# Performance work log

Measured on AMD Instinct MI355X. Metric: run time of the kernel, lower is better.

## Reference

```python
import jax, jax.numpy as jnp
import numpy as np

B, D, V, S = 16384, 768, 50257, 100


def setup_inputs() -> dict:
    key = jax.random.key(0)
    k1, k2, k3, k4, k5 = jax.random.split(key, 5)
    return {
        "predictions": jax.random.normal(k1, (B, D), dtype=jnp.float32),
        "labels": jax.random.randint(k2, (B,), 0, V, dtype=jnp.int64)
        if jax.config.jax_enable_x64 else jax.random.randint(k2, (B,), 0, V).astype(jnp.int32),
        "projection": jax.random.normal(k3, (V, D), dtype=jnp.float32) * 0.02,
        "bias": jax.random.normal(k4, (V,), dtype=jnp.float32) * 0.02,
        "samples": jax.random.randint(k5, (S,), 0, V).astype(jnp.int32),
    }


def reference(predictions, labels, projection, bias, samples):
    n_classes = projection.shape[0]
    num_sampling = samples.shape[0]
    # true-label scores: gather rows then rowwise dot  [B]
    label_scores = jnp.einsum("bd,bd->b", predictions, projection[labels]) + bias[labels]
    # noise scores vs sampled classes  [B, S]
    noise_scores = predictions @ projection[samples].T + bias[samples][None, :]
    noise_scores = noise_scores + jnp.log(jnp.float32(n_classes - 1))
    # reject accidental hits of the true label among samples
    reject = (labels[:, None] == samples[None, :]) & (labels[:, None] != -100)
    noise_scores = noise_scores - 1000000.0 * reject.astype(noise_scores.dtype)
    noise_scores = noise_scores - jnp.log(
        (num_sampling - reject.sum(-1, keepdims=True)).astype(jnp.float32)
    )
    scores = jnp.concatenate([label_scores[:, None], noise_scores], axis=-1)  # [B, 1+S]
    # cross_entropy with target class 0, ignore_index -100 semantics
    valid = labels != -100
    per_tok = -jax.nn.log_softmax(scores, axis=-1)[:, 0]
    n_valid = jnp.maximum(valid.sum(), 1)
    loss = jnp.sum(jnp.where(valid, per_tok, 0.0)) / n_valid.astype(per_tok.dtype)
    return loss
```

## Files before the change

### kernel.cpp

```cpp
#include <hip/hip_runtime.h>
#include <hip/hip_bf16.h>
#include <math.h>

#define BM 16
#define SPAD 112
#define NTILE 7
#define NTHREADS 256

typedef __attribute__((ext_vector_type(8))) short short8;
typedef __attribute__((ext_vector_type(4))) float f32x4;

__device__ __forceinline__ unsigned short f2bfu(float f) {
    union { __hip_bfloat16 h; unsigned short u; } cv;
    cv.h = __float2bfloat16(f);
    return cv.u;
}

__global__ void ssce_qprep(const float* __restrict__ proj,
                           const int*   __restrict__ samples,
                           unsigned short* __restrict__ Qb, int D, int S)
{
    const int t    = blockIdx.x / 12;
    const int ck   = blockIdx.x % 12;
    const int tid  = threadIdx.x;
    const int lane = tid & 63;
    const int ks   = tid >> 6;
    const int col  = lane & 15;
    const int g    = lane >> 4;

    int s   = t * 16 + col;
    int row = samples[s < S ? s : S - 1];
    const float* src = proj + (size_t)row * D + ck * 64 + ks * 32 + g * 8;
    unsigned short* dst = Qb + ((size_t)((t * 12 + ck) * 2 + ks) * 64 + lane) * 8;
    #pragma unroll
    for (int e = 0; e < 8; ++e) dst[e] = f2bfu(src[e]);
}

__global__ __launch_bounds__(NTHREADS)
void ssce_main(const float* __restrict__ pred,
               const int*   __restrict__ labels,
               const float* __restrict__ proj,
               const float* __restrict__ bias,
               const int*   __restrict__ samples,
               const unsigned short* __restrict__ Qb,
               float* __restrict__ partials,
               int Btot, int D, int S, float logV1)
{
    __shared__ unsigned short sAb[2][BM][128];
    __shared__ float scores[BM * 113];
    __shared__ float sLabelScore[BM];
    __shared__ float sBiasS[SPAD];
    __shared__ int   sSamp[SPAD];
    __shared__ int   sLabels[BM];
    __shared__ float sPt[4], sVc[4];

    const int tid  = threadIdx.x;
    const int lane = tid & 63;
    const int w    = tid >> 6;
    const int l16  = lane & 15;
    const int g    = lane >> 4;
    const int ctA  = 2 * w;
    const int ctB  = (w == 3) ? 6 : 2 * w + 1;
    const int rowBase = blockIdx.x * BM;

    if (tid < SPAD) {
        int s = (tid < S) ? samples[tid] : -1;
        sSamp[tid]  = s;
        sBiasS[tid] = (s >= 0) ? bias[s] : 0.0f;
    }
    if (tid < BM) {
        int gr = rowBase + tid;
        sLabels[tid] = (gr < Btot) ? labels[gr] : -100;
    }
    __syncthreads();

    const int sr = tid >> 4;
    const int li = tid & 15;
    const float* aSrc = pred + (size_t)min(rowBase + sr, Btot - 1) * D + li * 4;
    const int lab_sr  = sLabels[sr];
    const float lflag = (lab_sr >= 0) ? 1.0f : 0.0f;
    const float* lSrc = proj + (size_t)(lab_sr >= 0 ? lab_sr : 0) * D + li * 4;

    const int swz = sr & 7;
    const int wByteLo = sr * 256 + ((((li >> 1) ^ swz)      ) << 4) + ((li & 1) << 3);
    const int wByteHi = sr * 256 + ((((li >> 1) ^ swz) + 8  ) << 4) + ((li & 1) << 3);
    int rByte[4];
    #pragma unroll
    for (int ks = 0; ks < 4; ++ks)
        rByte[ks] = l16 * 256 + (((ks * 4 + g) ^ (l16 & 7)) << 4);

    const unsigned short* qA = Qb + ((size_t)(ctA * 24) * 64 + lane) * 8;
    const unsigned short* qB = Qb + ((size_t)(ctB * 24) * 64 + lane) * 8;

    f32x4 acc0 = {0.f,0.f,0.f,0.f}, acc1 = {0.f,0.f,0.f,0.f};
    float lpart = 0.0f;

    const int nIt = D >> 7;

    float4 pf0 = *(const float4*)(aSrc);
    float4 pf1 = *(const float4*)(aSrc + 64);
    float4 pl0 = *(const float4*)(lSrc);
    float4 pl1 = *(const float4*)(lSrc + 64);

    char* ldsBase = (char*)&sAb[0][0][0];

    for (int it = 0; it < nIt; ++it) {
        const int kk   = it << 7;
        const int boff = (it & 1) * (BM * 256);

        unsigned int u0 = (unsigned)f2bfu(pf0.x) | ((unsigned)f2bfu(pf0.y) << 16);
        unsigned int u1 = (unsigned)f2bfu(pf0.z) | ((unsigned)f2bfu(pf0.w) << 16);
        unsigned int u2 = (unsigned)f2bfu(pf1.x) | ((unsigned)f2bfu(pf1.y) << 16);
        unsigned int u3 = (unsigned)f2bfu(pf1.z) | ((unsigned)f2bfu(pf1.w) << 16);
        *(uint2*)(ldsBase + boff + wByteLo) = make_uint2(u0, u1);
        *(uint2*)(ldsBase + boff + wByteHi) = make_uint2(u2, u3);

        lpart += pf0.x * pl0.x + pf0.y * pl0.y + pf0.z * pl0.z + pf0.w * pl0.w;
        lpart += pf1.x * pl1.x + pf1.y * pl1.y + pf1.z * pl1.z + pf1.w * pl1.w;

        __syncthreads();

        if (it + 1 < nIt) {
            pf0 = *(const float4*)(aSrc + kk + 128);
            pf1 = *(const float4*)(aSrc + kk + 192);
            pl0 = *(const float4*)(lSrc + kk + 128);
            pl1 = *(const float4*)(lSrc + kk + 192);
        }

        const size_t fo = (size_t)(it * 4) * 512;
        short8 bA[4], bB[4];
        #pragma unroll
        for (int ks = 0; ks < 4; ++ks) {
            bA[ks] = *(const short8*)(qA + fo + ks * 512);
            bB[ks] = *(const short8*)(qB + fo + ks * 512);
        }

        #pragma unroll
        for (int ks = 0; ks < 4; ++ks) {
            short8 a8 = *(const short8*)(ldsBase + boff + rByte[ks]);
            acc0 = __builtin_amdgcn_mfma_f32_16x16x32_bf16(a8, bA[ks], acc0, 0, 0, 0);
            acc1 = __builtin_amdgcn_mfma_f32_16x16x32_bf16(a8, bB[ks], acc1, 0, 0, 0);
        }
    }

    lpart *= lflag;
    lpart += __shfl_down(lpart, 8, 16);
    lpart += __shfl_down(lpart, 4, 16);
    lpart += __shfl_down(lpart, 2, 16);
    lpart += __shfl_down(lpart, 1, 16);
    if (li == 0)
        sLabelScore[sr] = (lab_sr >= 0) ? (lpart + bias[lab_sr]) : 0.0f;

    #pragma unroll
    for (int i = 0; i < 4; ++i) {
        int row = g * 4 + i;
        scores[row * 113 + ctA * 16 + l16] = acc0[i];
        scores[row * 113 + ctB * 16 + l16] = acc1[i];
    }
    __syncthreads();

    const int  row   = sr;
    const int  lab   = lab_sr;
    const bool valid = (lab != -100) && (rowBase + row < Btot);

    int cnt = 0;
    #pragma unroll
    for (int k = 0; k < 7; ++k) {
        int s = li + 16 * k;
        if (s < S) cnt += (sSamp[s] == lab) ? 1 : 0;
    }
    cnt += __shfl_xor(cnt, 1, 16);
    cnt += __shfl_xor(cnt, 2, 16);
    cnt += __shfl_xor(cnt, 4, 16);
    cnt += __shfl_xor(cnt, 8, 16);

    const float corr = logV1 - __logf((float)(S - cnt));
    const float ls   = sLabelScore[row];

    float v7[7];
    float mv = -1e30f;
    #pragma unroll
    for (int k = 0; k < 7; ++k) {
        int s = li + 16 * k;
        float v = -1e30f;
        if (s < S) {
            v = scores[row * 113 + s] + sBiasS[s] + corr;
            if (valid && sSamp[s] == lab) v -= 1000000.0f;
        }
        v7[k] = v;
        mv = fmaxf(mv, v);
    }
    mv = fmaxf(mv, __shfl_xor(mv, 1, 16));
    mv = fmaxf(mv, __shfl_xor(mv, 2, 16));
    mv = fmaxf(mv, __shfl_xor(mv, 4, 16));
    mv = fmaxf(mv, __shfl_xor(mv, 8, 16));
    const float m = fmaxf(mv, ls);

    float se = 0.0f;
    #pragma unroll
    for (int k = 0; k < 7; ++k)
        se += __expf(v7[k] - m);
    se += __shfl_xor(se, 1, 16);
    se += __shfl_xor(se, 2, 16);
    se += __shfl_xor(se, 4, 16);
    se += __shfl_xor(se, 8, 16);

    float pt = 0.0f, vc = 0.0f;
    if (li == 0 && valid) {
        float set = se + __expf(ls - m);
        pt = m - ls + __logf(set);
        vc = 1.0f;
    }
    pt += __shfl_down(pt, 16); vc += __shfl_down(vc, 16);
    pt += __shfl_down(pt, 32); vc += __shfl_down(vc, 32);
    if (lane == 0) { sPt[w] = pt; sVc[w] = vc; }
    __syncthreads();
    if (tid == 0) {
        float P = sPt[0] + sPt[1] + sPt[2] + sPt[3];
        float C = sVc[0] + sVc[1] + sVc[2] + sVc[3];
        partials[blockIdx.x]             = P;
        partials[gridDim.x + blockIdx.x] = C;
    }
}

__global__ void ssce_final(const float* __restrict__ partials, int nb,
                           float* __restrict__ out)
{
    __shared__ float red[8];
    int tid = threadIdx.x;
    float s = 0.0f, c = 0.0f;
    for (int i = tid; i < nb; i += 256) {
        s += partials[i];
        c += partials[nb + i];
    }
    #pragma unroll
    for (int off = 32; off > 0; off >>= 1) {
        s += __shfl_down(s, off);
        c += __shfl_down(c, off);
    }
    int wv = tid >> 6;
    if ((tid & 63) == 0) { red[wv * 2] = s; red[wv * 2 + 1] = c; }
    __syncthreads();
    if (tid == 0) {
        float S2 = 0.0f, C2 = 0.0f;
        for (int i = 0; i < 4; ++i) { S2 += red[i * 2]; C2 += red[i * 2 + 1]; }
        out[0] = S2 / fmaxf(C2, 1.0f);
    }
}

extern "C" void kernel_launch(void* const* d_in, const int* in_sizes, int n_in,
                              void* d_out, int out_size, void* d_ws, size_t ws_size,
                              hipStream_t stream)
{
    const float* pred    = (const float*)d_in[0];
    const int*   labels  = (const int*)  d_in[1];
    const float* proj    = (const float*)d_in[2];
    const float* bias    = (const float*)d_in[3];
    const int*   samples = (const int*)  d_in[4];

    const int B = in_sizes[1];
    const int V = in_sizes[3];
    const int S = in_sizes[4];
    const int D = in_sizes[0] / B;

    float logV1 = logf((float)(V - 1));
    float* partials = (float*)d_ws;
    unsigned short* Qb = (unsigned short*)((char*)d_ws + 16384);

    ssce_qprep<<<NTILE * 12, 128, 0, stream>>>(proj, samples, Qb, D, S);

    const int grid = (B + BM - 1) / BM;
    ssce_main<<<grid, NTHREADS, 0, stream>>>(pred, labels, proj, bias, samples,
                                             Qb, partials, B, D, S, logV1);
    ssce_final<<<1, 256, 0, stream>>>(partials, grid, (float*)d_out);
}
```

Before: 33.51 us.

## Unroll K loop by two and prefetch deeper for A and B operands

Restructures the main K loop into a 2x-unrolled ping-pong that keeps two stages of prediction and label-row data in flight. It also prefetches the next iteration's B fragments from the precomputed bf16 Q buffer before the current MFMAs run. The aim is to hide global load latency behind MFMA work, which the single-stage loop exposed. The cost is higher register pressure, and the loop assumes nIt is even (D/128 = 6 here).

```diff
diff --git a/kernel.cpp b/kernel.cpp
--- a/kernel.cpp
+++ b/kernel.cpp
@@ -35,6 +35,38 @@
     #pragma unroll
     for (int e = 0; e < 8; ++e) dst[e] = f2bfu(src[e]);
 }
+
+#define DOT4(a, b) ((a).x*(b).x + (a).y*(b).y + (a).z*(b).z + (a).w*(b).w)
+
+#define STAGEW(BOFF, P0, P1)                                                  \
+  {                                                                           \
+    unsigned int u0 = (unsigned)f2bfu((P0).x) | ((unsigned)f2bfu((P0).y)<<16);\
+    unsigned int u1 = (unsigned)f2bfu((P0).z) | ((unsigned)f2bfu((P0).w)<<16);\
+    unsigned int u2 = (unsigned)f2bfu((P1).x) | ((unsigned)f2bfu((P1).y)<<16);\
+    unsigned int u3 = (unsigned)f2bfu((P1).z) | ((unsigned)f2bfu((P1).w)<<16);\
+    *(uint2*)(ldsBase + (BOFF) + wByteLo) = make_uint2(u0, u1);               \
+    *(uint2*)(ldsBase + (BOFF) + wByteHi) = make_uint2(u2, u3);               \
+  }
+
+#define LOADB(DA, DB, IT)                                                     \
+  {                                                                           \
+    const size_t fo_ = (size_t)((IT) * 4) * 512;                              \
+    _Pragma("unroll")                                                         \
+    for (int ks = 0; ks < 4; ++ks) {                                          \
+      DA[ks] = *(const short8*)(qA + fo_ + ks * 512);                         \
+      DB[ks] = *(const short8*)(qB + fo_ + ks * 512);                         \
+    }                                                                         \
+  }
+
+#define MFMAS(BA, BB, BOFF)                                                   \
+  {                                                                           \
+    _Pragma("unroll")                                                         \
+    for (int ks = 0; ks < 4; ++ks) {                                          \
+      short8 a8 = *(const short8*)(ldsBase + (BOFF) + rByte[ks]);             \
+      acc0 = __builtin_amdgcn_mfma_f32_16x16x32_bf16(a8, BA[ks], acc0, 0,0,0);\
+      acc1 = __builtin_amdgcn_mfma_f32_16x16x32_bf16(a8, BB[ks], acc1, 0,0,0);\
+    }                                                                         \
+  }
 
 __global__ __launch_bounds__(NTHREADS)
 void ssce_main(const float* __restrict__ pred,
@@ -82,8 +114,8 @@
     const float* lSrc = proj + (size_t)(lab_sr >= 0 ? lab_sr : 0) * D + li * 4;
 
     const int swz = sr & 7;
-    const int wByteLo = sr * 256 + ((((li >> 1) ^ swz)      ) << 4) + ((li & 1) << 3);
-    const int wByteHi = sr * 256 + ((((li >> 1) ^ swz) + 8  ) << 4) + ((li & 1) << 3);
+    const int wByteLo = sr * 256 + ((((li >> 1) ^ swz)     ) << 4) + ((li & 1) << 3);
+    const int wByteHi = sr * 256 + ((((li >> 1) ^ swz) + 8 ) << 4) + ((li & 1) << 3);
     int rByte[4];
     #pragma unroll
     for (int ks = 0; ks < 4; ++ks)
@@ -96,51 +128,46 @@
     float lpart = 0.0f;
 
     const int nIt = D >> 7;
-
-    float4 pf0 = *(const float4*)(aSrc);
-    float4 pf1 = *(const float4*)(aSrc + 64);
-    float4 pl0 = *(const float4*)(lSrc);
-    float4 pl1 = *(const float4*)(lSrc + 64);
-
     char* ldsBase = (char*)&sAb[0][0][0];
 
-    for (int it = 0; it < nIt; ++it) {
-        const int kk   = it << 7;
-        const int boff = (it & 1) * (BM * 256);
-
-        unsigned int u0 = (unsigned)f2bfu(pf0.x) | ((unsigned)f2bfu(pf0.y) << 16);
-        unsigned int u1 = (unsigned)f2bfu(pf0.z) | ((unsigned)f2bfu(pf0.w) << 16);
-        unsigned int u2 = (unsigned)f2bfu(pf1.x) | ((unsigned)f2bfu(pf1.y) << 16);
-        unsigned int u3 = (unsigned)f2bfu(pf1.z) | ((unsigned)f2bfu(pf1.w) << 16);
-        *(uint2*)(ldsBase + boff + wByteLo) = make_uint2(u0, u1);
-        *(uint2*)(ldsBase + boff + wByteHi) = make_uint2(u2, u3);
-
-        lpart += pf0.x * pl0.x + pf0.y * pl0.y + pf0.z * pl0.z + pf0.w * pl0.w;
-        lpart += pf1.x * pl1.x + pf1.y * pl1.y + pf1.z * pl1.z + pf1.w * pl1.w;
-
+    float4 pfA0 = *(const float4*)(aSrc);
+    float4 pfA1 = *(const float4*)(aSrc + 64);
+    float4 plA0 = *(const float4*)(lSrc);
+    float4 plA1 = *(const float4*)(lSrc + 64);
+    float4 pfB0 = *(const float4*)(aSrc + 128);
+    float4 pfB1 = *(const float4*)(aSrc + 192);
+    float4 plB0 = *(const float4*)(lSrc + 128);
+    float4 plB1 = *(const float4*)(lSrc + 192);
+
+    short8 bEA[4], bEB[4], bOA[4], bOB[4];
+    LOADB(bEA, bEB, 0);
+
+    for (int it = 0; it < nIt; it += 2) {
+        STAGEW(0, pfA0, pfA1);
+        lpart += DOT4(pfA0, plA0) + DOT4(pfA1, plA1);
         __syncthreads();
-
-        if (it + 1 < nIt) {
-            pf0 = *(const float4*)(aSrc + kk + 128);
-            pf1 = *(const float4*)(aSrc + kk + 192);
-            pl0 = *(const float4*)(lSrc + kk + 128);
-            pl1 = *(const float4*)(lSrc + kk + 192);
+        if (it + 2 < nIt) {
+            const int k2 = (it + 2) << 7;
+            pfA0 = *(const float4*)(aSrc + k2);
+            pfA1 = *(const float4*)(aSrc + k2 + 64);
+            plA0 = *(const float4*)(lSrc + k2);
+            plA1 = *(const float4*)(lSrc + k2 + 64);
         }
-
-        const size_t fo = (size_t)(it * 4) * 512;
-        short8 bA[4], bB[4];
-        #pragma unroll
-        for (int ks = 0; ks < 4; ++ks) {
-            bA[ks] = *(const short8*)(qA + fo + ks * 512);
-            bB[ks] = *(const short8*)(qB + fo + ks * 512);
+        LOADB(bOA, bOB, it + 1);
+        MFMAS(bEA, bEB, 0);
+
+        STAGEW(4096, pfB0, pfB1);
+        lpart += DOT4(pfB0, plB0) + DOT4(pfB1, plB1);
+        __syncthreads();
+        if (it + 3 < nIt) {
+            const int k3 = (it + 3) << 7;
+            pfB0 = *(const float4*)(aSrc + k3);
+            pfB1 = *(const float4*)(aSrc + k3 + 64);
+            plB0 = *(const float4*)(lSrc + k3);
+            plB1 = *(const float4*)(lSrc + k3 + 64);
         }
-
-        #pragma unroll
-        for (int ks = 0; ks < 4; ++ks) {
-            short8 a8 = *(const short8*)(ldsBase + boff + rByte[ks]);
-            acc0 = __builtin_amdgcn_mfma_f32_16x16x32_bf16(a8, bA[ks], acc0, 0, 0, 0);
-            acc1 = __builtin_amdgcn_mfma_f32_16x16x32_bf16(a8, bB[ks], acc1, 0, 0, 0);
-        }
+        if (it + 2 < nIt) LOADB(bEA, bEB, it + 2);
+        MFMAS(bOA, bOB, 4096);
     }
 
     lpart *= lflag;
```

Result: no change. 33.69 us (+0.5%).

## Halve rows per block to eight, padding MFMA A tile with zeros

Applied to the files above, without the earlier changes.

Each block now handles 8 rows instead of 16, which doubles the grid so more blocks run across CUs. Each row is loaded by 32 threads instead of 16, and rows 8-15 of the LDS A tile are zero-filled so the 16x16 MFMA shape stays the same. The cost is that half of the MFMA work is wasted and every block re-reads the full Q fragments, doubling Q traffic from L2. The partials workspace offset is moved to fit the larger grid.

```diff
diff --git a/kernel.cpp b/kernel.cpp
--- a/kernel.cpp
+++ b/kernel.cpp
@@ -2,7 +2,7 @@
 #include <hip/hip_bf16.h>
 #include <math.h>
 
-#define BM 16
+#define BM 8
 #define SPAD 112
 #define NTILE 7
 #define NTHREADS 256
@@ -35,6 +35,8 @@
     #pragma unroll
     for (int e = 0; e < 8; ++e) dst[e] = f2bfu(src[e]);
 }
+
+#define DOT4(a, b) ((a).x*(b).x + (a).y*(b).y + (a).z*(b).z + (a).w*(b).w)
 
 __global__ __launch_bounds__(NTHREADS)
 void ssce_main(const float* __restrict__ pred,
@@ -46,7 +48,7 @@
                float* __restrict__ partials,
                int Btot, int D, int S, float logV1)
 {
-    __shared__ unsigned short sAb[2][BM][128];
+    __shared__ unsigned short sAb[2][16][128];
     __shared__ float scores[BM * 113];
     __shared__ float sLabelScore[BM];
     __shared__ float sBiasS[SPAD];
@@ -72,18 +74,23 @@
         int gr = rowBase + tid;
         sLabels[tid] = (gr < Btot) ? labels[gr] : -100;
     }
-    __syncthreads();
-
-    const int sr = tid >> 4;
-    const int li = tid & 15;
-    const float* aSrc = pred + (size_t)min(rowBase + sr, Btot - 1) * D + li * 4;
+    {
+        int buf = tid >> 7;
+        int idx = tid & 127;
+        char* z = (char*)&sAb[buf][8][0] + idx * 16;
+        *(uint4*)z = make_uint4(0u, 0u, 0u, 0u);
+    }
+    __syncthreads();
+
+    const int sr   = tid >> 5;
+    const int li32 = tid & 31;
+    const float* aSrc = pred + (size_t)min(rowBase + sr, Btot - 1) * D + li32 * 4;
     const int lab_sr  = sLabels[sr];
     const float lflag = (lab_sr >= 0) ? 1.0f : 0.0f;
-    const float* lSrc = proj + (size_t)(lab_sr >= 0 ? lab_sr : 0) * D + li * 4;
+    const float* lSrc = proj + (size_t)(lab_sr >= 0 ? lab_sr : 0) * D + li32 * 4;
 
     const int swz = sr & 7;
-    const int wByteLo = sr * 256 + ((((li >> 1) ^ swz)      ) << 4) + ((li & 1) << 3);
-    const int wByteHi = sr * 256 + ((((li >> 1) ^ swz) + 8  ) << 4) + ((li & 1) << 3);
+    const int wByte = sr * 256 + ((((li32 >> 1) ^ swz)) << 4) + ((li32 & 1) << 3);
     int rByte[4];
     #pragma unroll
     for (int ks = 0; ks < 4; ++ks)
@@ -96,35 +103,26 @@
     float lpart = 0.0f;
 
     const int nIt = D >> 7;
-
-    float4 pf0 = *(const float4*)(aSrc);
-    float4 pf1 = *(const float4*)(aSrc + 64);
-    float4 pl0 = *(const float4*)(lSrc);
-    float4 pl1 = *(const float4*)(lSrc + 64);
-
     char* ldsBase = (char*)&sAb[0][0][0];
+
+    float4 pf = *(const float4*)(aSrc);
+    float4 pl = *(const float4*)(lSrc);
 
     for (int it = 0; it < nIt; ++it) {
         const int kk   = it << 7;
-        const int boff = (it & 1) * (BM * 256);
-
-        unsigned int u0 = (unsigned)f2bfu(pf0.x) | ((unsigned)f2bfu(pf0.y) << 16);
-        unsigned int u1 = (unsigned)f2bfu(pf0.z) | ((unsigned)f2bfu(pf0.w) << 16);
-        unsigned int u2 = (unsigned)f2bfu(pf1.x) | ((unsigned)f2bfu(pf1.y) << 16);
-        unsigned int u3 = (unsigned)f2bfu(pf1.z) | ((unsigned)f2bfu(pf1.w) << 16);
-        *(uint2*)(ldsBase + boff + wByteLo) = make_uint2(u0, u1);
-        *(uint2*)(ldsBase + boff + wByteHi) = make_uint2(u2, u3);
-
-        lpart += pf0.x * pl0.x + pf0.y * pl0.y + pf0.z * pl0.z + pf0.w * pl0.w;
-        lpart += pf1.x * pl1.x + pf1.y * pl1.y + pf1.z * pl1.z + pf1.w * pl1.w;
+        const int boff = (it & 1) * 4096;
+
+        unsigned int u0 = (unsigned)f2bfu(pf.x) | ((unsigned)f2bfu(pf.y) << 16);
+        unsigned int u1 = (unsigned)f2bfu(pf.z) | ((unsigned)f2bfu(pf.w) << 16);
+        *(uint2*)(ldsBase + boff + wByte) = make_uint2(u0, u1);
+
+        lpart += DOT4(pf, pl);
 
         __syncthreads();
 
         if (it + 1 < nIt) {
-            pf0 = *(const float4*)(aSrc + kk + 128);
-            pf1 = *(const float4*)(aSrc + kk + 192);
-            pl0 = *(const float4*)(lSrc + kk + 128);
-            pl1 = *(const float4*)(lSrc + kk + 192);
+            pf = *(const float4*)(aSrc + kk + 128);
+            pl = *(const float4*)(lSrc + kk + 128);
         }
 
         const size_t fo = (size_t)(it * 4) * 512;
@@ -144,82 +142,88 @@
     }
 
     lpart *= lflag;
-    lpart += __shfl_down(lpart, 8, 16);
-    lpart += __shfl_down(lpart, 4, 16);
-    lpart += __shfl_down(lpart, 2, 16);
-    lpart += __shfl_down(lpart, 1, 16);
-    if (li == 0)
+    lpart += __shfl_down(lpart, 16, 32);
+    lpart += __shfl_down(lpart,  8, 32);
+    lpart += __shfl_down(lpart,  4, 32);
+    lpart += __shfl_down(lpart,  2, 32);
+    lpart += __shfl_down(lpart,  1, 32);
+    if (li32 == 0)
         sLabelScore[sr] = (lab_sr >= 0) ? (lpart + bias[lab_sr]) : 0.0f;
 
-    #pragma unroll
-    for (int i = 0; i < 4; ++i) {
-        int row = g * 4 + i;
-        scores[row * 113 + ctA * 16 + l16] = acc0[i];
-        scores[row * 113 + ctB * 16 + l16] = acc1[i];
-    }
-    __syncthreads();
-
-    const int  row   = sr;
-    const int  lab   = lab_sr;
-    const bool valid = (lab != -100) && (rowBase + row < Btot);
-
-    int cnt = 0;
-    #pragma unroll
-    for (int k = 0; k < 7; ++k) {
-        int s = li + 16 * k;
-        if (s < S) cnt += (sSamp[s] == lab) ? 1 : 0;
-    }
-    cnt += __shfl_xor(cnt, 1, 16);
-    cnt += __shfl_xor(cnt, 2, 16);
-    cnt += __shfl_xor(cnt, 4, 16);
-    cnt += __shfl_xor(cnt, 8, 16);
-
-    const float corr = logV1 - __logf((float)(S - cnt));
-    const float ls   = sLabelScore[row];
-
-    float v7[7];
-    float mv = -1e30f;
-    #pragma unroll
-    for (int k = 0; k < 7; ++k) {
-        int s = li + 16 * k;
-        float v = -1e30f;
-        if (s < S) {
-            v = scores[row * 113 + s] + sBiasS[s] + corr;
-            if (valid && sSamp[s] == lab) v -= 1000000.0f;
-        }
-        v7[k] = v;
-        mv = fmaxf(mv, v);
-    }
-    mv = fmaxf(mv, __shfl_xor(mv, 1, 16));
-    mv = fmaxf(mv, __shfl_xor(mv, 2, 16));
-    mv = fmaxf(mv, __shfl_xor(mv, 4, 16));
-    mv = fmaxf(mv, __shfl_xor(mv, 8, 16));
-    const float m = fmaxf(mv, ls);
-
-    float se = 0.0f;
-    #pragma unroll
-    for (int k = 0; k < 7; ++k)
-        se += __expf(v7[k] - m);
-    se += __shfl_xor(se, 1, 16);
-    se += __shfl_xor(se, 2, 16);
-    se += __shfl_xor(se, 4, 16);
-    se += __shfl_xor(se, 8, 16);
+    if (g < 2) {
+        #pragma unroll
+        for (int i = 0; i < 4; ++i) {
+            int row = g * 4 + i;
+            scores[row * 113 + ctA * 16 + l16] = acc0[i];
+            scores[row * 113 + ctB * 16 + l16] = acc1[i];
+        }
+    }
+    __syncthreads();
+
+    const int gid = tid >> 4;
+    const int li  = tid & 15;
 
     float pt = 0.0f, vc = 0.0f;
-    if (li == 0 && valid) {
-        float set = se + __expf(ls - m);
-        pt = m - ls + __logf(set);
-        vc = 1.0f;
+    if (gid < BM) {
+        const int  row   = gid;
+        const int  lab   = sLabels[row];
+        const bool valid = (lab != -100) && (rowBase + row < Btot);
+
+        int cnt = 0;
+        #pragma unroll
+        for (int k = 0; k < 7; ++k) {
+            int s = li + 16 * k;
+            if (s < S) cnt += (sSamp[s] == lab) ? 1 : 0;
+        }
+        cnt += __shfl_xor(cnt, 1, 16);
+        cnt += __shfl_xor(cnt, 2, 16);
+        cnt += __shfl_xor(cnt, 4, 16);
+        cnt += __shfl_xor(cnt, 8, 16);
+
+        const float corr = logV1 - __logf((float)(S - cnt));
+        const float ls   = sLabelScore[row];
+
+        float v7[7];
+        float mv = -1e30f;
+        #pragma unroll
+        for (int k = 0; k < 7; ++k) {
+            int s = li + 16 * k;
+            float v = -1e30f;
+            if (s < S) {
+                v = scores[row * 113 + s] + sBiasS[s] + corr;
+                if (valid && sSamp[s] == lab) v -= 1000000.0f;
+            }
+            v7[k] = v;
+            mv = fmaxf(mv, v);
+        }
+        mv = fmaxf(mv, __shfl_xor(mv, 1, 16));
+        mv = fmaxf(mv, __shfl_xor(mv, 2, 16));
+        mv = fmaxf(mv, __shfl_xor(mv, 4, 16));
+        mv = fmaxf(mv, __shfl_xor(mv, 8, 16));
+        const float m = fmaxf(mv, ls);
+
+        float se = 0.0f;
+        #pragma unroll
+        for (int k = 0; k < 7; ++k)
+            se += __expf(v7[k] - m);
+        se += __shfl_xor(se, 1, 16);
+        se += __shfl_xor(se, 2, 16);
+        se += __shfl_xor(se, 4, 16);
+        se += __shfl_xor(se, 8, 16);
+
+        if (li == 0 && valid) {
+            float set = se + __expf(ls - m);
+            pt = m - ls + __logf(set);
+            vc = 1.0f;
+        }
     }
     pt += __shfl_down(pt, 16); vc += __shfl_down(vc, 16);
     pt += __shfl_down(pt, 32); vc += __shfl_down(vc, 32);
     if (lane == 0) { sPt[w] = pt; sVc[w] = vc; }
     __syncthreads();
     if (tid == 0) {
-        float P = sPt[0] + sPt[1] + sPt[2] + sPt[3];
-        float C = sVc[0] + sVc[1] + sVc[2] + sVc[3];
-        partials[blockIdx.x]             = P;
-        partials[gridDim.x + blockIdx.x] = C;
+        partials[blockIdx.x]             = sPt[0] + sPt[1] + sPt[2] + sPt[3];
+        partials[gridDim.x + blockIdx.x] = sVc[0] + sVc[1] + sVc[2] + sVc[3];
     }
 }
 
@@ -265,7 +269,7 @@
 
     float logV1 = logf((float)(V - 1));
     float* partials = (float*)d_ws;
-    unsigned short* Qb = (unsigned short*)((char*)d_ws + 16384);
+    unsigned short* Qb = (unsigned short*)((char*)d_ws + 32768);
 
     ssce_qprep<<<NTILE * 12, 128, 0, stream>>>(proj, samples, Qb, D, S);
 
```

New measurement: 41.53 us. +23.9%, slower.

## Stage full A tile into LDS up front, drop per-iteration barriers

Applied to the files above, without the earlier changes.

Instead of double-buffering 128-wide K chunks with a barrier every iteration, all six chunks of the prediction rows are converted to bf16 and written to LDS in one prologue. Two loads are kept in flight, and a single __syncthreads follows before the MFMA loop runs. The aim is to remove five block-wide barriers and let global loads overlap more freely. The cost is 6x more LDS for the A tile, which may reduce occupancy. The code also hardcodes six chunks, so it assumes D=768. The workspace offset for Qb is moved as well.

```diff
diff --git a/kernel.cpp b/kernel.cpp
--- a/kernel.cpp
+++ b/kernel.cpp
@@ -35,6 +35,18 @@
     #pragma unroll
     for (int e = 0; e < 8; ++e) dst[e] = f2bfu(src[e]);
 }
+
+#define DOT4(a, b) ((a).x*(b).x + (a).y*(b).y + (a).z*(b).z + (a).w*(b).w)
+
+#define STAGEW(BOFF, P0, P1)                                                  \
+  {                                                                           \
+    unsigned int u0 = (unsigned)f2bfu((P0).x) | ((unsigned)f2bfu((P0).y)<<16);\
+    unsigned int u1 = (unsigned)f2bfu((P0).z) | ((unsigned)f2bfu((P0).w)<<16);\
+    unsigned int u2 = (unsigned)f2bfu((P1).x) | ((unsigned)f2bfu((P1).y)<<16);\
+    unsigned int u3 = (unsigned)f2bfu((P1).z) | ((unsigned)f2bfu((P1).w)<<16);\
+    *(uint2*)(ldsBase + (BOFF) + wByteLo) = make_uint2(u0, u1);               \
+    *(uint2*)(ldsBase + (BOFF) + wByteHi) = make_uint2(u2, u3);               \
+  }
 
 __global__ __launch_bounds__(NTHREADS)
 void ssce_main(const float* __restrict__ pred,
@@ -46,7 +58,7 @@
                float* __restrict__ partials,
                int Btot, int D, int S, float logV1)
 {
-    __shared__ unsigned short sAb[2][BM][128];
+    __shared__ unsigned short sAb[6][BM][128];
     __shared__ float scores[BM * 113];
     __shared__ float sLabelScore[BM];
     __shared__ float sBiasS[SPAD];
@@ -82,8 +94,8 @@
     const float* lSrc = proj + (size_t)(lab_sr >= 0 ? lab_sr : 0) * D + li * 4;
 
     const int swz = sr & 7;
-    const int wByteLo = sr * 256 + ((((li >> 1) ^ swz)      ) << 4) + ((li & 1) << 3);
-    const int wByteHi = sr * 256 + ((((li >> 1) ^ swz) + 8  ) << 4) + ((li & 1) << 3);
+    const int wByteLo = sr * 256 + ((((li >> 1) ^ swz)     ) << 4) + ((li & 1) << 3);
+    const int wByteHi = sr * 256 + ((((li >> 1) ^ swz) + 8 ) << 4) + ((li & 1) << 3);
     int rByte[4];
     #pragma unroll
     for (int ks = 0; ks < 4; ++ks)
@@ -95,46 +107,52 @@
     f32x4 acc0 = {0.f,0.f,0.f,0.f}, acc1 = {0.f,0.f,0.f,0.f};
     float lpart = 0.0f;
 
+    char* ldsBase = (char*)&sAb[0][0][0];
+
+    {
+        float4 pA0 = *(const float4*)(aSrc);
+        float4 pA1 = *(const float4*)(aSrc + 64);
+        float4 lA0 = *(const float4*)(lSrc);
+        float4 lA1 = *(const float4*)(lSrc + 64);
+        float4 pB0 = *(const float4*)(aSrc + 128);
+        float4 pB1 = *(const float4*)(aSrc + 192);
+        float4 lB0 = *(const float4*)(lSrc + 128);
+        float4 lB1 = *(const float4*)(lSrc + 192);
+
+        for (int c = 0; c < 6; c += 2) {
+            STAGEW(c * 4096, pA0, pA1);
+            lpart += DOT4(pA0, lA0) + DOT4(pA1, lA1);
+            if (c + 2 < 6) {
+                const int k2 = (c + 2) << 7;
+                pA0 = *(const float4*)(aSrc + k2);
+                pA1 = *(const float4*)(aSrc + k2 + 64);
+                lA0 = *(const float4*)(lSrc + k2);
+                lA1 = *(const float4*)(lSrc + k2 + 64);
+            }
+            STAGEW((c + 1) * 4096, pB0, pB1);
+            lpart += DOT4(pB0, lB0) + DOT4(pB1, lB1);
+            if (c + 3 < 6) {
+                const int k3 = (c + 3) << 7;
+                pB0 = *(const float4*)(aSrc + k3);
+                pB1 = *(const float4*)(aSrc + k3 + 64);
+                lB0 = *(const float4*)(lSrc + k3);
+                lB1 = *(const float4*)(lSrc + k3 + 64);
+            }
+        }
+    }
+    __syncthreads();
+
     const int nIt = D >> 7;
-
-    float4 pf0 = *(const float4*)(aSrc);
-    float4 pf1 = *(const float4*)(aSrc + 64);
-    float4 pl0 = *(const float4*)(lSrc);
-    float4 pl1 = *(const float4*)(lSrc + 64);
-
-    char* ldsBase = (char*)&sAb[0][0][0];
-
     for (int it = 0; it < nIt; ++it) {
-        const int kk   = it << 7;
-        const int boff = (it & 1) * (BM * 256);
-
-        unsigned int u0 = (unsigned)f2bfu(pf0.x) | ((unsigned)f2bfu(pf0.y) << 16);
-        unsigned int u1 = (unsigned)f2bfu(pf0.z) | ((unsigned)f2bfu(pf0.w) << 16);
-        unsigned int u2 = (unsigned)f2bfu(pf1.x) | ((unsigned)f2bfu(pf1.y) << 16);
-        unsigned int u3 = (unsigned)f2bfu(pf1.z) | ((unsigned)f2bfu(pf1.w) << 16);
-        *(uint2*)(ldsBase + boff + wByteLo) = make_uint2(u0, u1);
-        *(uint2*)(ldsBase + boff + wByteHi) = make_uint2(u2, u3);
-
-        lpart += pf0.x * pl0.x + pf0.y * pl0.y + pf0.z * pl0.z + pf0.w * pl0.w;
-        lpart += pf1.x * pl1.x + pf1.y * pl1.y + pf1.z * pl1.z + pf1.w * pl1.w;
-
-        __syncthreads();
-
-        if (it + 1 < nIt) {
-            pf0 = *(const float4*)(aSrc + kk + 128);
-            pf1 = *(const float4*)(aSrc + kk + 192);
-            pl0 = *(const float4*)(lSrc + kk + 128);
-            pl1 = *(const float4*)(lSrc + kk + 192);
-        }
-
+        const int boff = it * 4096;
         const size_t fo = (size_t)(it * 4) * 512;
+
         short8 bA[4], bB[4];
         #pragma unroll
         for (int ks = 0; ks < 4; ++ks) {
             bA[ks] = *(const short8*)(qA + fo + ks * 512);
             bB[ks] = *(const short8*)(qB + fo + ks * 512);
         }
-
         #pragma unroll
         for (int ks = 0; ks < 4; ++ks) {
             short8 a8 = *(const short8*)(ldsBase + boff + rByte[ks]);
@@ -216,10 +234,8 @@
     if (lane == 0) { sPt[w] = pt; sVc[w] = vc; }
     __syncthreads();
     if (tid == 0) {
-        float P = sPt[0] + sPt[1] + sPt[2] + sPt[3];
-        float C = sVc[0] + sVc[1] + sVc[2] + sVc[3];
-        partials[blockIdx.x]             = P;
-        partials[gridDim.x + blockIdx.x] = C;
+        partials[blockIdx.x]             = sPt[0] + sPt[1] + sPt[2] + sPt[3];
+        partials[gridDim.x + blockIdx.x] = sVc[0] + sVc[1] + sVc[2] + sVc[3];
     }
 }
 
@@ -265,7 +281,7 @@
 
     float logV1 = logf((float)(V - 1));
     float* partials = (float*)d_ws;
-    unsigned short* Qb = (unsigned short*)((char*)d_ws + 16384);
+    unsigned short* Qb = (unsigned short*)((char*)d_ws + 32768);
 
     ssce_qprep<<<NTILE * 12, 128, 0, stream>>>(proj, samples, Qb, D, S);
 
```

Result: slower. 39.51 us (+17.9%).
